# Kernel tuning notes

Hardware: AMD Instinct MI355X
Metric: run time of the kernel (lower is better)

## Reference

```python
import jax, jax.numpy as jnp
import numpy as np

N = 100000   # nodes
E = 600000   # edges
D = 128      # d_model
R = 200      # num_relations


def setup_inputs() -> dict:
    key = jax.random.key(0)
    ks = jax.random.split(key, 12)
    def nrm(k, shape, scale=0.02):
        return jax.random.normal(k, shape, jnp.float32) * scale
    return dict(
        node_features=jax.random.normal(ks[0], (N, D), jnp.float32),
        edge_index=jax.random.randint(ks[1], (2, E), 0, N),
        edge_type=jax.random.randint(ks[2], (E,), 0, R),
        rel_embed=nrm(ks[3], (R, D)),
        msg_w1=nrm(ks[4], (2 * D, D)), msg_b1=jnp.zeros((D,), jnp.float32),
        msg_w2=nrm(ks[5], (D, D)), msg_b2=jnp.zeros((D,), jnp.float32),
        attn_w1=nrm(ks[6], (2 * D, D)), attn_b1=jnp.zeros((D,), jnp.float32),
        attn_w2=nrm(ks[7], (D, 1)), attn_b2=jnp.zeros((1,), jnp.float32),
        ln1_g=jnp.ones((D,), jnp.float32), ln1_b=jnp.zeros((D,), jnp.float32),
        ffn_w1=nrm(ks[8], (D, 4 * D)), ffn_b1=jnp.zeros((4 * D,), jnp.float32),
        ffn_w2=nrm(ks[9], (4 * D, D)), ffn_b2=jnp.zeros((D,), jnp.float32),
        ln2_g=jnp.ones((D,), jnp.float32), ln2_b=jnp.zeros((D,), jnp.float32),
    )


def layer_norm(x, g, b, eps=1e-5):
    mu = x.mean(-1, keepdims=True)
    var = ((x - mu) ** 2).mean(-1, keepdims=True)
    return (x - mu) * jax.lax.rsqrt(var + eps) * g + b


def reference(node_features, edge_index, edge_type, rel_embed,
              msg_w1, msg_b1, msg_w2, msg_b2,
              attn_w1, attn_b1, attn_w2, attn_b2,
              ln1_g, ln1_b, ffn_w1, ffn_b1, ffn_w2, ffn_b2,
              ln2_g, ln2_b):
    Nn = node_features.shape[0]
    src, dst = edge_index[0], edge_index[1]
    # gather + edge message MLP
    src_feat = node_features[src]              # [E, D]
    rel_feat = rel_embed[edge_type]            # [E, D]
    h = jnp.concatenate([src_feat, rel_feat], axis=-1)          # [E, 2D]
    messages = jax.nn.relu(h @ msg_w1 + msg_b1) @ msg_w2 + msg_b2  # [E, D]
    # edge attention logits
    a_in = jnp.concatenate([node_features[dst], messages], axis=-1)  # [E, 2D]
    attn_raw = (jax.nn.leaky_relu(a_in @ attn_w1 + attn_b1, 0.2) @ attn_w2 + attn_b2)[:, 0]  # [E]
    # two-pass segment softmax over destination nodes
    attn_max = jax.ops.segment_max(attn_raw, dst, num_segments=Nn)   # [N]
    attn_exp = jnp.exp(attn_raw - attn_max[dst])                      # [E]
    attn_sum = jax.ops.segment_sum(attn_exp, dst, num_segments=Nn)   # [N]
    attn_w = attn_exp / (attn_sum[dst] + 1e-8)                        # [E]
    # scatter-add weighted messages
    aggr = jax.ops.segment_sum(attn_w[:, None] * messages, dst, num_segments=Nn)  # [N, D]
    x = layer_norm(node_features + aggr, ln1_g, ln1_b)
    ffn = jax.nn.gelu(x @ ffn_w1 + ffn_b1, approximate=False) @ ffn_w2 + ffn_b2
    return layer_norm(x + ffn, ln2_g, ln2_b)
```

## Files before the change

kernel.cpp:

```cpp
#include <hip/hip_runtime.h>
#include <hip/hip_bf16.h>

#define NN 100000
#define NE 600000
#define DD 128
#define RR 200
#define SCAN_NB ((NN + 255) / 256)

typedef __attribute__((ext_vector_type(8))) short bf16x8;
typedef __attribute__((ext_vector_type(4))) float f32x4;

__device__ __forceinline__ unsigned int bfbits(float x) {
    return (unsigned int)__builtin_bit_cast(unsigned short, __float2bfloat16(x));
}
__device__ __forceinline__ unsigned int pk2(float a, float b) {
    return bfbits(a) | (bfbits(b) << 16);
}
__device__ __forceinline__ unsigned short bf16s(float x) {
    return __builtin_bit_cast(unsigned short, __float2bfloat16(x));
}
__device__ __forceinline__ float unbf(unsigned short u) {
    return __builtin_bit_cast(float, ((unsigned int)u) << 16);
}
__device__ __forceinline__ float unlo(unsigned int u) {
    return __builtin_bit_cast(float, u << 16);
}
__device__ __forceinline__ float unhi(unsigned int u) {
    return __builtin_bit_cast(float, u & 0xffff0000u);
}

__device__ __forceinline__ void gload_lds16(const void* g, void* l) {
    __builtin_amdgcn_global_load_lds(
        (const __attribute__((address_space(1))) void*)g,
        (__attribute__((address_space(3))) void*)l, 16, 0, 0);
}

__global__ void k_initc(int* __restrict__ cnt) {
    int i = blockIdx.x * 256 + threadIdx.x;
    if (i < NN) cnt[i] = 0;
}

__global__ void k_hist(const int* __restrict__ dst, int* __restrict__ cnt) {
    int e = blockIdx.x * 256 + threadIdx.x;
    if (e < NE) atomicAdd(&cnt[dst[e]], 1);
}

__global__ void k_scanA(const int* __restrict__ cnt, int* __restrict__ bsum) {
    __shared__ int red[256];
    int i = blockIdx.x * 256 + threadIdx.x;
    red[threadIdx.x] = (i < NN) ? cnt[i] : 0;
    __syncthreads();
    for (int off = 128; off >= 1; off >>= 1) {
        if (threadIdx.x < off) red[threadIdx.x] += red[threadIdx.x + off];
        __syncthreads();
    }
    if (threadIdx.x == 0) bsum[blockIdx.x] = red[0];
}

__global__ void k_scanB(int* __restrict__ bsum) {
    __shared__ int sh[512];
    int t = threadIdx.x;
    int v = (t < SCAN_NB) ? bsum[t] : 0;
    sh[t] = v;
    __syncthreads();
    for (int off = 1; off < 512; off <<= 1) {
        int add = (t >= off) ? sh[t - off] : 0;
        __syncthreads();
        sh[t] += add;
        __syncthreads();
    }
    if (t < SCAN_NB) bsum[t] = sh[t] - v;
}

__global__ void k_scanC(const int* __restrict__ cnt, const int* __restrict__ bsum,
                        int* __restrict__ row_start, int* __restrict__ cursor) {
    __shared__ int sh[256];
    int i = blockIdx.x * 256 + threadIdx.x;
    int t = threadIdx.x;
    int v = (i < NN) ? cnt[i] : 0;
    sh[t] = v;
    __syncthreads();
    for (int off = 1; off < 256; off <<= 1) {
        int add = (t >= off) ? sh[t - off] : 0;
        __syncthreads();
        sh[t] += add;
        __syncthreads();
    }
    if (i < NN) {
        int ex = bsum[blockIdx.x] + sh[t] - v;
        row_start[i] = ex;
        cursor[i] = ex;
    }
}

__global__ void k_bucket(const int* __restrict__ src, const int* __restrict__ dst,
                         const int* __restrict__ etype, int* __restrict__ cursor,
                         int* __restrict__ srcs, int* __restrict__ ets,
                         int* __restrict__ dsts) {
    int e = blockIdx.x * 256 + threadIdx.x;
    if (e < NE) {
        int d = dst[e];
        int p = atomicAdd(&cursor[d], 1);
        srcs[p] = src[e];
        ets[p]  = etype[e];
        dsts[p] = d;
    }
}

__global__ void k_prep(const float* __restrict__ nf, unsigned short* __restrict__ nfb) {
    int i = blockIdx.x * 256 + threadIdx.x;
    if (i >= NN * DD / 8) return;
    const float* sp = nf + (size_t)i * 8;
    float4 f0 = *reinterpret_cast<const float4*>(sp);
    float4 f1 = *reinterpret_cast<const float4*>(sp + 4);
    uint4 v;
    v.x = pk2(f0.x, f0.y); v.y = pk2(f0.z, f0.w);
    v.z = pk2(f1.x, f1.y); v.w = pk2(f1.z, f1.w);
    *reinterpret_cast<uint4*>(nfb + (size_t)i * 8) = v;
}

__global__ void k_setup(const float* __restrict__ mw1, const float* __restrict__ mb1,
                        const float* __restrict__ mw2, const float* __restrict__ mb2,
                        const float* __restrict__ aw1, const float* __restrict__ rel,
                        const float* __restrict__ fw1, const float* __restrict__ fw2,
                        unsigned short* __restrict__ mw1p,
                        unsigned short* __restrict__ mw2p,
                        unsigned short* __restrict__ awTp,
                        unsigned short* __restrict__ mwBp,
                        unsigned short* __restrict__ fw1p,
                        unsigned short* __restrict__ fw2p,
                        unsigned short* __restrict__ relcb,
                        float* __restrict__ zb) {
    int idx = blockIdx.x * 256 + threadIdx.x;
    if (idx < 16384) {
        int i = idx & 7, l = (idx >> 3) & 63, ks = (idx >> 9) & 3, nt = idx >> 11;
        int k = ks * 32 + (l >> 4) * 8 + i, n = nt * 16 + (l & 15);
        mw1p[idx] = bf16s(mw1[k * 128 + n]);
    } else if (idx < 32768) {
        int j = idx - 16384;
        int i = j & 7, l = (j >> 3) & 63, ks = (j >> 9) & 3, nt = j >> 11;
        int k = ks * 32 + (l >> 4) * 8 + i, n = nt * 16 + (l & 15);
        mw2p[j] = bf16s(mw2[k * 128 + n]);
    } else if (idx < 49152) {
        int j = idx - 32768;
        int i = j & 7, l = (j >> 3) & 63, ks = (j >> 9) & 3, nt = j >> 11;
        int k = ks * 32 + (l >> 4) * 8 + i, n = nt * 16 + (l & 15);
        awTp[j] = bf16s(aw1[k * 128 + n]);
    } else if (idx < 65536) {
        int j = idx - 49152;
        int i = j & 7, l = (j >> 3) & 63, ks = (j >> 9) & 3, nt = j >> 11;
        int k = ks * 32 + (l >> 4) * 8 + i, n = nt * 16 + (l & 15);
        float s = 0.0f;
        for (int j2 = 0; j2 < 128; ++j2)
            s = fmaf(mw2[k * 128 + j2], aw1[(128 + j2) * 128 + n], s);
        mwBp[j] = bf16s(s);
    } else if (idx < 131072) {
        int j = idx - 65536;
        int i = j & 7, l = (j >> 3) & 63, ks = (j >> 9) & 3, nt = j >> 11;
        int k = ks * 32 + (l >> 4) * 8 + i, n = nt * 16 + (l & 15);
        fw1p[j] = bf16s(fw1[k * 512 + n]);
    } else if (idx < 196608) {
        int j = idx - 131072;
        int i = j & 7, l = (j >> 3) & 63, ks = (j >> 9) & 15, nt = j >> 13;
        int k = ks * 32 + (l >> 4) * 8 + i, n = nt * 16 + (l & 15);
        fw2p[j] = bf16s(fw2[k * 128 + n]);
    } else if (idx < 222208) {
        int j = idx - 196608;
        int r = j >> 7, n = j & 127;
        float s = mb1[n];
        for (int k = 0; k < 128; ++k)
            s = fmaf(rel[r * 128 + k], mw1[(128 + k) * 128 + n], s);
        relcb[j] = bf16s(s);
    } else if (idx < 222336) {
        int n = idx - 222208;
        float s = 0.0f;
        for (int j2 = 0; j2 < 128; ++j2)
            s = fmaf(mb2[j2], aw1[(128 + j2) * 128 + n], s);
        zb[n] = s;
    }
}

__global__ __launch_bounds__(256) void k_nfa(
    const unsigned short* __restrict__ nfb, const unsigned short* __restrict__ awTp,
    const float* __restrict__ ab1, unsigned short* __restrict__ nfa)
{
    __shared__ alignas(16) unsigned short XB[64 * 128];
    const int t = threadIdx.x;
    const int w = t >> 6, l = t & 63;
    const int wm = w >> 1, wn = w & 1;
    const int lm = l & 15, lk = l >> 4;
    const int lrow = l >> 4, lslot = l & 15;
    const int n0 = blockIdx.x * 64;

    #pragma unroll
    for (int it = 0; it < 4; ++it) {
        int rb = w * 16 + it * 4;
        int row = rb + lrow;
        long grow = n0 + row; if (grow >= NN) grow = NN - 1;
        int c = lslot ^ (row & 7);
        gload_lds16(nfb + grow * DD + c * 8, &XB[rb * 128]);
    }
    __syncthreads();

    f32x4 acc[2][4];
    #pragma unroll
    for (int mf = 0; mf < 2; ++mf)
        #pragma unroll
        for (int nfr = 0; nfr < 4; ++nfr) acc[mf][nfr] = (f32x4){0.f, 0.f, 0.f, 0.f};

    #pragma unroll
    for (int ks = 0; ks < 4; ++ks) {
        bf16x8 a[2];
        #pragma unroll
        for (int mf = 0; mf < 2; ++mf) {
            int m = wm * 32 + mf * 16 + lm;
            int slot = (ks * 4 + lk) ^ (m & 7);
            a[mf] = *reinterpret_cast<const bf16x8*>(&XB[m * 128 + slot * 8]);
        }
        #pragma unroll
        for (int nfr = 0; nfr < 4; ++nfr) {
            int nt = wn * 4 + nfr;
            bf16x8 b = *reinterpret_cast<const bf16x8*>(&awTp[((nt * 4 + ks) * 64 + l) * 8]);
            acc[0][nfr] = __builtin_amdgcn_mfma_f32_16x16x32_bf16(a[0], b, acc[0][nfr], 0, 0, 0);
            acc[1][nfr] = __builtin_amdgcn_mfma_f32_16x16x32_bf16(a[1], b, acc[1][nfr], 0, 0, 0);
        }
    }
    __syncthreads();

    #pragma unroll
    for (int nfr = 0; nfr < 4; ++nfr) {
        int n = wn * 64 + nfr * 16 + lm;
        float bv = ab1[n];
        #pragma unroll
        for (int mf = 0; mf < 2; ++mf)
            #pragma unroll
            for (int r = 0; r < 4; ++r) {
                int m = wm * 32 + mf * 16 + lk * 4 + r;
                XB[m * 128 + n] = bf16s(acc[mf][nfr][r] + bv);
            }
    }
    __syncthreads();

    #pragma unroll
    for (int j = 0; j < 4; ++j) {
        int q = j * 256 + t;
        int row = q >> 4, c16 = q & 15;
        if (n0 + row < NN)
            *reinterpret_cast<uint4*>(&nfa[(size_t)(n0 + row) * DD + c16 * 8]) =
                *reinterpret_cast<const uint4*>(&XB[row * 128 + c16 * 8]);
    }
}

__global__ __launch_bounds__(512) void k_edge(
    const unsigned short* __restrict__ nfb, const int* __restrict__ srcs,
    const int* __restrict__ dsts, const int* __restrict__ ets,
    const unsigned short* __restrict__ nfa, const unsigned short* __restrict__ relcb,
    const unsigned short* __restrict__ mw1p, const unsigned short* __restrict__ mwBp,
    const float* __restrict__ zb, const float* __restrict__ aw2,
    const float* __restrict__ ab2,
    unsigned short* __restrict__ hid_out, float* __restrict__ attn_raw)
{
    __shared__ alignas(16) unsigned short S[64 * 128];
    __shared__ alignas(16) unsigned short H[64 * 128];
    __shared__ float RED[64][4];

    const int t = threadIdx.x;
    const int w = t >> 6, l = t & 63;
    const int wm = w >> 2, wn = w & 3;
    const int lm = l & 15, lk = l >> 4;
    const int lrow = l >> 4, lslot = l & 15;
    const int e0 = blockIdx.x * 64;

    #pragma unroll
    for (int it = 0; it < 2; ++it) {
        int rb = w * 8 + it * 4;
        int row = rb + lrow;
        int c = lslot ^ (row & 7);
        gload_lds16(nfb + (size_t)srcs[e0 + row] * DD + c * 8, &S[rb * 128]);
    }
    #pragma unroll
    for (int it = 0; it < 2; ++it) {
        int rb = w * 8 + it * 4;
        int row = rb + lrow;
        int c = lslot ^ (row & 7);
        gload_lds16(relcb + (size_t)ets[e0 + row] * DD + c * 8, &H[rb * 128]);
    }
    __syncthreads();

    {
        f32x4 acc1[2][2];
        #pragma unroll
        for (int mf = 0; mf < 2; ++mf)
            #pragma unroll
            for (int nfr = 0; nfr < 2; ++nfr) acc1[mf][nfr] = (f32x4){0.f, 0.f, 0.f, 0.f};

        #pragma unroll
        for (int ks = 0; ks < 4; ++ks) {
            bf16x8 a[2];
            #pragma unroll
            for (int mf = 0; mf < 2; ++mf) {
                int m = wm * 32 + mf * 16 + lm;
                int slot = (ks * 4 + lk) ^ (m & 7);
                a[mf] = *reinterpret_cast<const bf16x8*>(&S[m * 128 + slot * 8]);
            }
            #pragma unroll
            for (int nfr = 0; nfr < 2; ++nfr) {
                int nt = wn * 2 + nfr;
                bf16x8 b = *reinterpret_cast<const bf16x8*>(&mw1p[((nt * 4 + ks) * 64 + l) * 8]);
                acc1[0][nfr] = __builtin_amdgcn_mfma_f32_16x16x32_bf16(a[0], b, acc1[0][nfr], 0, 0, 0);
                acc1[1][nfr] = __builtin_amdgcn_mfma_f32_16x16x32_bf16(a[1], b, acc1[1][nfr], 0, 0, 0);
            }
        }
        #pragma unroll
        for (int nfr = 0; nfr < 2; ++nfr) {
            int n = (wn * 2 + nfr) * 16 + lm;
            #pragma unroll
            for (int mf = 0; mf < 2; ++mf)
                #pragma unroll
                for (int r = 0; r < 4; ++r) {
                    int m = wm * 32 + mf * 16 + lk * 4 + r;
                    int sl = m * 128 + ((n >> 3) ^ (m & 7)) * 8 + (n & 7);
                    float v = acc1[mf][nfr][r] + unbf(H[sl]);
                    v = fmaxf(v, 0.0f);
                    H[sl] = bf16s(v);
                }
        }
    }
    __syncthreads();

    #pragma unroll
    for (int j = 0; j < 2; ++j) {
        int q = j * 512 + t;
        int row = q >> 4, c16 = q & 15;
        int slot = c16 ^ (row & 7);
        *reinterpret_cast<uint4*>(&hid_out[(size_t)(e0 + row) * DD + c16 * 8]) =
            *reinterpret_cast<const uint4*>(&H[row * 128 + slot * 8]);
    }
    #pragma unroll
    for (int it = 0; it < 2; ++it) {
        int rb = w * 8 + it * 4;
        int row = rb + lrow;
        int c = lslot ^ (row & 7);
        gload_lds16(nfa + (size_t)dsts[e0 + row] * DD + c * 8, &S[rb * 128]);
    }

    f32x4 acc[2][2];
    #pragma unroll
    for (int mf = 0; mf < 2; ++mf)
        #pragma unroll
        for (int nfr = 0; nfr < 2; ++nfr) acc[mf][nfr] = (f32x4){0.f, 0.f, 0.f, 0.f};

    #pragma unroll
    for (int ks = 0; ks < 4; ++ks) {
        bf16x8 a[2];
        #pragma unroll
        for (int mf = 0; mf < 2; ++mf) {
            int m = wm * 32 + mf * 16 + lm;
            int slot = (ks * 4 + lk) ^ (m & 7);
            a[mf] = *reinterpret_cast<const bf16x8*>(&H[m * 128 + slot * 8]);
        }
        #pragma unroll
        for (int nfr = 0; nfr < 2; ++nfr) {
            int nt = wn * 2 + nfr;
            bf16x8 b = *reinterpret_cast<const bf16x8*>(&mwBp[((nt * 4 + ks) * 64 + l) * 8]);
            acc[0][nfr] = __builtin_amdgcn_mfma_f32_16x16x32_bf16(a[0], b, acc[0][nfr], 0, 0, 0);
            acc[1][nfr] = __builtin_amdgcn_mfma_f32_16x16x32_bf16(a[1], b, acc[1][nfr], 0, 0, 0);
        }
    }
    __syncthreads();

    {
        float zbv[2], aw2v[2];
        #pragma unroll
        for (int nfr = 0; nfr < 2; ++nfr) {
            int nc = (wn * 2 + nfr) * 16 + lm;
            zbv[nfr] = zb[nc];
            aw2v[nfr] = aw2[nc];
        }
        #pragma unroll
        for (int mf = 0; mf < 2; ++mf)
            #pragma unroll
            for (int r = 0; r < 4; ++r) {
                int m = wm * 32 + mf * 16 + lk * 4 + r;
                float s = 0.0f;
                #pragma unroll
                for (int nfr = 0; nfr < 2; ++nfr) {
                    int nc = (wn * 2 + nfr) * 16 + lm;
                    float v = acc[mf][nfr][r] + zbv[nfr]
                            + unbf(S[m * 128 + ((nc >> 3) ^ (m & 7)) * 8 + (nc & 7)]);
                    v = (v > 0.0f) ? v : 0.2f * v;
                    s = fmaf(v, aw2v[nfr], s);
                }
                s += __shfl_xor(s, 1, 64);
                s += __shfl_xor(s, 2, 64);
                s += __shfl_xor(s, 4, 64);
                s += __shfl_xor(s, 8, 64);
                if (lm == 0) RED[m][wn] = s;
            }
    }
    __syncthreads();

    if (t < 64) {
        attn_raw[e0 + t] = RED[t][0] + RED[t][1] + RED[t][2] + RED[t][3] + ab2[0];
    }
}

__global__ __launch_bounds__(256) void k_aggr(
    const unsigned short* __restrict__ hid, const float* __restrict__ raw,
    const int* __restrict__ row_start, const int* __restrict__ cnt,
    unsigned short* __restrict__ haggrb)
{
    const int l = threadIdx.x & 63;
    const int n = blockIdx.x * 4 + (threadIdx.x >> 6);
    if (n >= NN) return;
    const int rs = row_start[n], deg = cnt[n];

    float m = -INFINITY;
    for (int j = l; j < deg; j += 64) m = fmaxf(m, raw[rs + j]);
    #pragma unroll
    for (int off = 32; off >= 1; off >>= 1) m = fmaxf(m, __shfl_xor(m, off, 64));

    float s = 0.0f;
    for (int j = l; j < deg; j += 64) s += expf(raw[rs + j] - m);
    #pragma unroll
    for (int off = 32; off >= 1; off >>= 1) s += __shfl_xor(s, off, 64);
    const float rinv = 1.0f / (s + 1e-8f);

    float a0 = 0.0f, a1 = 0.0f;
    for (int j = 0; j < deg; ++j) {
        float w = expf(raw[rs + j] - m) * rinv;
        unsigned int v = *reinterpret_cast<const unsigned int*>(
            &hid[(size_t)(rs + j) * DD + l * 2]);
        a0 = fmaf(w, unlo(v), a0);
        a1 = fmaf(w, unhi(v), a1);
    }
    *reinterpret_cast<unsigned int*>(&haggrb[(size_t)n * DD + l * 2]) = pk2(a0, a1);
}

__global__ __launch_bounds__(512) void k_node(
    const float* __restrict__ nf, const unsigned short* __restrict__ haggrb,
    const unsigned short* __restrict__ mw2p, const float* __restrict__ mb2,
    const float* __restrict__ g1, const float* __restrict__ b1,
    const unsigned short* __restrict__ fw1p, const float* __restrict__ fb1,
    const unsigned short* __restrict__ fw2p, const float* __restrict__ fb2,
    const float* __restrict__ g2, const float* __restrict__ b2,
    float* __restrict__ out)
{
    __shared__ alignas(16) unsigned short XB[64 * 128];
    __shared__ alignas(16) unsigned short HB[64 * 256];

    const int t = threadIdx.x;
    const int w = t >> 6, l = t & 63;
    const int wm = w >> 2, wn = w & 3;
    const int lm = l & 15, lk = l >> 4;
    const int lrow = l >> 4, lslot = l & 15;
    const int row = t >> 3;
    const int q = t & 7;
    const long n0 = (long)blockIdx.x * 64;
    const long rg = n0 + row;
    const long rc = (rg < NN) ? rg : (NN - 1);

    unsigned short* HG = HB;
    #pragma unroll
    for (int it = 0; it < 2; ++it) {
        int rb = w * 8 + it * 4;
        int rr = rb + lrow;
        long grow = n0 + rr; if (grow >= NN) grow = NN - 1;
        int c = lslot ^ (rr & 7);
        gload_lds16(haggrb + grow * DD + c * 8, &HG[rb * 128]);
    }
    __syncthreads();

    {
        f32x4 acc0[2][2];
        #pragma unroll
        for (int mf = 0; mf < 2; ++mf)
            #pragma unroll
            for (int nfr = 0; nfr < 2; ++nfr) acc0[mf][nfr] = (f32x4){0.f, 0.f, 0.f, 0.f};

        #pragma unroll
        for (int ks = 0; ks < 4; ++ks) {
            bf16x8 a[2];
            #pragma unroll
            for (int mf = 0; mf < 2; ++mf) {
                int m = wm * 32 + mf * 16 + lm;
                int slot = (ks * 4 + lk) ^ (m & 7);
                a[mf] = *reinterpret_cast<const bf16x8*>(&HG[m * 128 + slot * 8]);
            }
            #pragma unroll
            for (int nfr = 0; nfr < 2; ++nfr) {
                int nt = wn * 2 + nfr;
                bf16x8 b = *reinterpret_cast<const bf16x8*>(&mw2p[((nt * 4 + ks) * 64 + l) * 8]);
                acc0[0][nfr] = __builtin_amdgcn_mfma_f32_16x16x32_bf16(a[0], b, acc0[0][nfr], 0, 0, 0);
                acc0[1][nfr] = __builtin_amdgcn_mfma_f32_16x16x32_bf16(a[1], b, acc0[1][nfr], 0, 0, 0);
            }
        }
        #pragma unroll
        for (int nfr = 0; nfr < 2; ++nfr) {
            int n = (wn * 2 + nfr) * 16 + lm;
            float bv = mb2[n];
            #pragma unroll
            for (int mf = 0; mf < 2; ++mf)
                #pragma unroll
                for (int r = 0; r < 4; ++r) {
                    int m = wm * 32 + mf * 16 + lk * 4 + r;
                    XB[m * 128 + ((n >> 3) ^ (m & 7)) * 8 + (n & 7)] = bf16s(acc0[mf][nfr][r] + bv);
                }
        }
    }
    __syncthreads();

    float xr[16];
    float s = 0.0f, ss = 0.0f;
    {
        const float* xp = nf + rc * DD + q * 16;
        #pragma unroll
        for (int i = 0; i < 2; ++i) {
            int c = q * 2 + i, slot = c ^ (row & 7);
            uint4 v = *reinterpret_cast<const uint4*>(&XB[row * 128 + slot * 8]);
            float f[8];
            f[0] = unlo(v.x); f[1] = unhi(v.x); f[2] = unlo(v.y); f[3] = unhi(v.y);
            f[4] = unlo(v.z); f[5] = unhi(v.z); f[6] = unlo(v.w); f[7] = unhi(v.w);
            float4 a = *reinterpret_cast<const float4*>(xp + i * 8);
            float4 b = *reinterpret_cast<const float4*>(xp + i * 8 + 4);
            float vv[8] = {a.x + f[0], a.y + f[1], a.z + f[2], a.w + f[3],
                           b.x + f[4], b.y + f[5], b.z + f[6], b.w + f[7]};
            #pragma unroll
            for (int j = 0; j < 8; ++j) {
                xr[i * 8 + j] = vv[j];
                s += vv[j];
                ss = fmaf(vv[j], vv[j], ss);
            }
        }
    }
    s  += __shfl_xor(s, 1, 64);  s  += __shfl_xor(s, 2, 64);  s  += __shfl_xor(s, 4, 64);
    ss += __shfl_xor(ss, 1, 64); ss += __shfl_xor(ss, 2, 64); ss += __shfl_xor(ss, 4, 64);
    {
        float mu = s * (1.0f / DD);
        float var = ss * (1.0f / DD) - mu * mu;
        float rstd = rsqrtf(var + 1e-5f);
        #pragma unroll
        for (int i = 0; i < 4; ++i) {
            float4 gv = *reinterpret_cast<const float4*>(g1 + q * 16 + i * 4);
            float4 bv = *reinterpret_cast<const float4*>(b1 + q * 16 + i * 4);
            xr[i * 4 + 0] = (xr[i * 4 + 0] - mu) * rstd * gv.x + bv.x;
            xr[i * 4 + 1] = (xr[i * 4 + 1] - mu) * rstd * gv.y + bv.y;
            xr[i * 4 + 2] = (xr[i * 4 + 2] - mu) * rstd * gv.z + bv.z;
            xr[i * 4 + 3] = (xr[i * 4 + 3] - mu) * rstd * gv.w + bv.w;
        }
        #pragma unroll
        for (int i = 0; i < 2; ++i) {
            int c = q * 2 + i, slot = c ^ (row & 7);
            uint4 v;
            v.x = pk2(xr[i * 8 + 0], xr[i * 8 + 1]);
            v.y = pk2(xr[i * 8 + 2], xr[i * 8 + 3]);
            v.z = pk2(xr[i * 8 + 4], xr[i * 8 + 5]);
            v.w = pk2(xr[i * 8 + 6], xr[i * 8 + 7]);
            *reinterpret_cast<uint4*>(&XB[row * 128 + slot * 8]) = v;
        }
    }
    __syncthreads();

    f32x4 acc2[2][2];
    #pragma unroll
    for (int mf = 0; mf < 2; ++mf)
        #pragma unroll
        for (int nfr = 0; nfr < 2; ++nfr) acc2[mf][nfr] = (f32x4){0.f, 0.f, 0.f, 0.f};

    #pragma unroll
    for (int half = 0; half < 2; ++half) {
        f32x4 acc[2][4];
        #pragma unroll
        for (int mf = 0; mf < 2; ++mf)
            #pragma unroll
            for (int nfr = 0; nfr < 4; ++nfr) acc[mf][nfr] = (f32x4){0.f, 0.f, 0.f, 0.f};

        #pragma unroll
        for (int ks = 0; ks < 4; ++ks) {
            bf16x8 a[2];
            #pragma unroll
            for (int mf = 0; mf < 2; ++mf) {
                int m = wm * 32 + mf * 16 + lm;
                int slot = (ks * 4 + lk) ^ (m & 7);
                a[mf] = *reinterpret_cast<const bf16x8*>(&XB[m * 128 + slot * 8]);
            }
            #pragma unroll
            for (int nfr = 0; nfr < 4; ++nfr) {
                int nt = half * 16 + wn * 4 + nfr;
                bf16x8 b = *reinterpret_cast<const bf16x8*>(&fw1p[((nt * 4 + ks) * 64 + l) * 8]);
                acc[0][nfr] = __builtin_amdgcn_mfma_f32_16x16x32_bf16(a[0], b, acc[0][nfr], 0, 0, 0);
                acc[1][nfr] = __builtin_amdgcn_mfma_f32_16x16x32_bf16(a[1], b, acc[1][nfr], 0, 0, 0);
            }
        }
        #pragma unroll
        for (int nfr = 0; nfr < 4; ++nfr) {
            int nl = (wn * 4 + nfr) * 16 + lm;
            float bv = fb1[half * 256 + nl];
            #pragma unroll
            for (int mf = 0; mf < 2; ++mf)
                #pragma unroll
                for (int r = 0; r < 4; ++r) {
                    int m = wm * 32 + mf * 16 + lk * 4 + r;
                    float h = acc[mf][nfr][r] + bv;
                    float e = __expf(h * -1.702f);
                    float gvv = h * __builtin_amdgcn_rcpf(1.0f + e);
                    HB[m * 256 + (((nl >> 3) ^ (m & 7)) * 8) + (nl & 7)] = bf16s(gvv);
                }
        }
        __syncthreads();

        #pragma unroll
        for (int ks = 0; ks < 8; ++ks) {
            bf16x8 a[2];
            #pragma unroll
            for (int mf = 0; mf < 2; ++mf) {
                int m = wm * 32 + mf * 16 + lm;
                int slot = (ks * 4 + lk) ^ (m & 7);
                a[mf] = *reinterpret_cast<const bf16x8*>(&HB[m * 256 + slot * 8]);
            }
            #pragma unroll
            for (int nfr = 0; nfr < 2; ++nfr) {
                int nt = wn * 2 + nfr;
                int kg = half * 8 + ks;
                bf16x8 b = *reinterpret_cast<const bf16x8*>(&fw2p[((nt * 16 + kg) * 64 + l) * 8]);
                acc2[0][nfr] = __builtin_amdgcn_mfma_f32_16x16x32_bf16(a[0], b, acc2[0][nfr], 0, 0, 0);
                acc2[1][nfr] = __builtin_amdgcn_mfma_f32_16x16x32_bf16(a[1], b, acc2[1][nfr], 0, 0, 0);
            }
        }
        __syncthreads();
    }

    #pragma unroll
    for (int nfr = 0; nfr < 2; ++nfr) {
        int n = (wn * 2 + nfr) * 16 + lm;
        float bv = fb2[n];
        #pragma unroll
        for (int mf = 0; mf < 2; ++mf)
            #pragma unroll
            for (int r = 0; r < 4; ++r) {
                int m = wm * 32 + mf * 16 + lk * 4 + r;
                XB[m * 128 + (((n >> 3) ^ (m & 7)) * 8) + (n & 7)] = bf16s(acc2[mf][nfr][r] + bv);
            }
    }
    __syncthreads();

    float s2 = 0.0f, ss2 = 0.0f;
    #pragma unroll
    for (int i = 0; i < 2; ++i) {
        int c = q * 2 + i, slot = c ^ (row & 7);
        uint4 v = *reinterpret_cast<const uint4*>(&XB[row * 128 + slot * 8]);
        float f[8];
        f[0] = unlo(v.x); f[1] = unhi(v.x); f[2] = unlo(v.y); f[3] = unhi(v.y);
        f[4] = unlo(v.z); f[5] = unhi(v.z); f[6] = unlo(v.w); f[7] = unhi(v.w);
        #pragma unroll
        for (int j = 0; j < 8; ++j) {
            float vv = xr[i * 8 + j] + f[j];
            xr[i * 8 + j] = vv;
            s2 += vv;
            ss2 = fmaf(vv, vv, ss2);
        }
    }
    s2  += __shfl_xor(s2, 1, 64);  s2  += __shfl_xor(s2, 2, 64);  s2  += __shfl_xor(s2, 4, 64);
    ss2 += __shfl_xor(ss2, 1, 64); ss2 += __shfl_xor(ss2, 2, 64); ss2 += __shfl_xor(ss2, 4, 64);
    {
        float mu = s2 * (1.0f / DD);
        float var = ss2 * (1.0f / DD) - mu * mu;
        float rstd = rsqrtf(var + 1e-5f);
        if (rg < NN) {
            float* op = out + rg * DD + q * 16;
            #pragma unroll
            for (int i = 0; i < 4; ++i) {
                float4 gv = *reinterpret_cast<const float4*>(g2 + q * 16 + i * 4);
                float4 bv = *reinterpret_cast<const float4*>(b2 + q * 16 + i * 4);
                float4 o;
                o.x = (xr[i * 4 + 0] - mu) * rstd * gv.x + bv.x;
                o.y = (xr[i * 4 + 1] - mu) * rstd * gv.y + bv.y;
                o.z = (xr[i * 4 + 2] - mu) * rstd * gv.z + bv.z;
                o.w = (xr[i * 4 + 3] - mu) * rstd * gv.w + bv.w;
                *reinterpret_cast<float4*>(op + i * 4) = o;
            }
        }
    }
}

extern "C" void kernel_launch(void* const* d_in, const int* in_sizes, int n_in,
                              void* d_out, int out_size, void* d_ws, size_t ws_size,
                              hipStream_t stream)
{
    const float* nf  = (const float*)d_in[0];
    const int*   ei  = (const int*)d_in[1];
    const int*   et  = (const int*)d_in[2];
    const float* rel = (const float*)d_in[3];
    const float* mw1 = (const float*)d_in[4];
    const float* mb1 = (const float*)d_in[5];
    const float* mw2 = (const float*)d_in[6];
    const float* mb2 = (const float*)d_in[7];
    const float* aw1 = (const float*)d_in[8];
    const float* ab1 = (const float*)d_in[9];
    const float* aw2 = (const float*)d_in[10];
    const float* ab2 = (const float*)d_in[11];
    const float* g1  = (const float*)d_in[12];
    const float* b1  = (const float*)d_in[13];
    const float* fw1 = (const float*)d_in[14];
    const float* fb1 = (const float*)d_in[15];
    const float* fw2 = (const float*)d_in[16];
    const float* fb2 = (const float*)d_in[17];
    const float* g2  = (const float*)d_in[18];
    const float* b2  = (const float*)d_in[19];
    float* out = (float*)d_out;

    char* ws = (char*)d_ws;
    size_t off = 0;
    auto alloc = [&](size_t bytes) -> char* {
        char* p = ws + off;
        off += (bytes + 255) & ~(size_t)255;
        return p;
    };
    unsigned short* hid = (unsigned short*)alloc((size_t)NE * DD * 2);
    float* attn_raw = (float*)alloc((size_t)NE * 4);
    unsigned short* haggrb = (unsigned short*)alloc((size_t)NN * DD * 2);
    unsigned short* nfb  = (unsigned short*)alloc((size_t)NN * DD * 2);
    unsigned short* relcb = (unsigned short*)alloc((size_t)RR * DD * 2);
    float* zb  = (float*)alloc((size_t)128 * 4);
    int* cnt       = (int*)alloc((size_t)NN * 4);
    int* row_start = (int*)alloc((size_t)NN * 4);
    int* cursor    = (int*)alloc((size_t)NN * 4);
    int* srcs      = (int*)alloc((size_t)NE * 4);
    int* ets       = (int*)alloc((size_t)NE * 4);
    int* dsts      = (int*)alloc((size_t)NE * 4);
    int* bsum      = (int*)alloc((size_t)SCAN_NB * 4);
    unsigned short* mw1p = (unsigned short*)alloc(16384 * 2);
    unsigned short* mw2p = (unsigned short*)alloc(16384 * 2);
    unsigned short* awTp = (unsigned short*)alloc(16384 * 2);
    unsigned short* mwBp = (unsigned short*)alloc(16384 * 2);
    unsigned short* fw1p = (unsigned short*)alloc(65536 * 2);
    unsigned short* fw2p = (unsigned short*)alloc(65536 * 2);

    unsigned short* nfa = haggrb;

    const int* srcp = ei;
    const int* dstp = ei + NE;

    hipLaunchKernelGGL(k_initc, dim3(SCAN_NB), dim3(256), 0, stream, cnt);
    hipLaunchKernelGGL(k_hist, dim3((NE + 255) / 256), dim3(256), 0, stream, dstp, cnt);
    hipLaunchKernelGGL(k_scanA, dim3(SCAN_NB), dim3(256), 0, stream, cnt, bsum);
    hipLaunchKernelGGL(k_scanB, dim3(1), dim3(512), 0, stream, bsum);
    hipLaunchKernelGGL(k_scanC, dim3(SCAN_NB), dim3(256), 0, stream, cnt, bsum, row_start, cursor);
    hipLaunchKernelGGL(k_bucket, dim3((NE + 255) / 256), dim3(256), 0, stream,
                       srcp, dstp, et, cursor, srcs, ets, dsts);
    hipLaunchKernelGGL(k_prep, dim3(NN * DD / 8 / 256), dim3(256), 0, stream, nf, nfb);
    hipLaunchKernelGGL(k_setup, dim3(869), dim3(256), 0, stream,
                       mw1, mb1, mw2, mb2, aw1, rel, fw1, fw2,
                       mw1p, mw2p, awTp, mwBp, fw1p, fw2p, relcb, zb);
    hipLaunchKernelGGL(k_nfa, dim3((NN + 63) / 64), dim3(256), 0, stream,
                       nfb, awTp, ab1, nfa);
    hipLaunchKernelGGL(k_edge, dim3(NE / 64), dim3(512), 0, stream,
                       nfb, srcs, dsts, ets, nfa, relcb,
                       mw1p, mwBp, zb, aw2, ab2,
                       hid, attn_raw);
    hipLaunchKernelGGL(k_aggr, dim3((NN + 3) / 4), dim3(256), 0, stream,
                       hid, attn_raw, row_start, cnt, haggrb);
    hipLaunchKernelGGL(k_node, dim3((NN + 63) / 64), dim3(512), 0, stream,
                       nf, haggrb, mw2p, mb2, g1, b1, fw1p, fb1, fw2p, fb2, g2, b2, out);
}
```

Before: 432.2 us.

## Fuse bf16 conversion into node-attention GEMM and aggregation into node kernel

Result: slower. 589.9 us (+36.5%).

```diff
diff --git a/kernel.cpp b/kernel.cpp
--- a/kernel.cpp
+++ b/kernel.cpp
@@ -105,18 +105,6 @@
         ets[p]  = etype[e];
         dsts[p] = d;
     }
-}
-
-__global__ void k_prep(const float* __restrict__ nf, unsigned short* __restrict__ nfb) {
-    int i = blockIdx.x * 256 + threadIdx.x;
-    if (i >= NN * DD / 8) return;
-    const float* sp = nf + (size_t)i * 8;
-    float4 f0 = *reinterpret_cast<const float4*>(sp);
-    float4 f1 = *reinterpret_cast<const float4*>(sp + 4);
-    uint4 v;
-    v.x = pk2(f0.x, f0.y); v.y = pk2(f0.z, f0.w);
-    v.z = pk2(f1.x, f1.y); v.w = pk2(f1.z, f1.w);
-    *reinterpret_cast<uint4*>(nfb + (size_t)i * 8) = v;
 }
 
 __global__ void k_setup(const float* __restrict__ mw1, const float* __restrict__ mb1,
@@ -180,25 +168,40 @@
     }
 }
 
-__global__ __launch_bounds__(256) void k_nfa(
-    const unsigned short* __restrict__ nfb, const unsigned short* __restrict__ awTp,
-    const float* __restrict__ ab1, unsigned short* __restrict__ nfa)
+__global__ __launch_bounds__(256) void k_prepnfa(
+    const float* __restrict__ nf, const unsigned short* __restrict__ awTp,
+    const float* __restrict__ ab1,
+    unsigned short* __restrict__ nfb, unsigned short* __restrict__ nfa)
 {
     __shared__ alignas(16) unsigned short XB[64 * 128];
     const int t = threadIdx.x;
     const int w = t >> 6, l = t & 63;
     const int wm = w >> 1, wn = w & 1;
     const int lm = l & 15, lk = l >> 4;
-    const int lrow = l >> 4, lslot = l & 15;
     const int n0 = blockIdx.x * 64;
 
-    #pragma unroll
-    for (int it = 0; it < 4; ++it) {
-        int rb = w * 16 + it * 4;
-        int row = rb + lrow;
-        long grow = n0 + row; if (grow >= NN) grow = NN - 1;
-        int c = lslot ^ (row & 7);
-        gload_lds16(nfb + grow * DD + c * 8, &XB[rb * 128]);
+    {
+        const int row = t >> 2, seg = t & 3;
+        long ng = n0 + row; if (ng >= NN) ng = NN - 1;
+        const float* sp = nf + ng * DD + seg * 32;
+        uint4 o[4];
+        #pragma unroll
+        for (int i = 0; i < 4; ++i) {
+            float4 f0 = *reinterpret_cast<const float4*>(sp + i * 8);
+            float4 f1 = *reinterpret_cast<const float4*>(sp + i * 8 + 4);
+            o[i].x = pk2(f0.x, f0.y); o[i].y = pk2(f0.z, f0.w);
+            o[i].z = pk2(f1.x, f1.y); o[i].w = pk2(f1.z, f1.w);
+        }
+        if (n0 + row < NN) {
+            #pragma unroll
+            for (int i = 0; i < 4; ++i)
+                *reinterpret_cast<uint4*>(&nfb[(size_t)(n0 + row) * DD + (seg * 4 + i) * 8]) = o[i];
+        }
+        #pragma unroll
+        for (int i = 0; i < 4; ++i) {
+            int c = seg * 4 + i, slot = c ^ (row & 7);
+            *reinterpret_cast<uint4*>(&XB[row * 128 + slot * 8]) = o[i];
+        }
     }
     __syncthreads();
 
@@ -405,40 +408,10 @@
     }
 }
 
-__global__ __launch_bounds__(256) void k_aggr(
-    const unsigned short* __restrict__ hid, const float* __restrict__ raw,
-    const int* __restrict__ row_start, const int* __restrict__ cnt,
-    unsigned short* __restrict__ haggrb)
-{
-    const int l = threadIdx.x & 63;
-    const int n = blockIdx.x * 4 + (threadIdx.x >> 6);
-    if (n >= NN) return;
-    const int rs = row_start[n], deg = cnt[n];
-
-    float m = -INFINITY;
-    for (int j = l; j < deg; j += 64) m = fmaxf(m, raw[rs + j]);
-    #pragma unroll
-    for (int off = 32; off >= 1; off >>= 1) m = fmaxf(m, __shfl_xor(m, off, 64));
-
-    float s = 0.0f;
-    for (int j = l; j < deg; j += 64) s += expf(raw[rs + j] - m);
-    #pragma unroll
-    for (int off = 32; off >= 1; off >>= 1) s += __shfl_xor(s, off, 64);
-    const float rinv = 1.0f / (s + 1e-8f);
-
-    float a0 = 0.0f, a1 = 0.0f;
-    for (int j = 0; j < deg; ++j) {
-        float w = expf(raw[rs + j] - m) * rinv;
-        unsigned int v = *reinterpret_cast<const unsigned int*>(
-            &hid[(size_t)(rs + j) * DD + l * 2]);
-        a0 = fmaf(w, unlo(v), a0);
-        a1 = fmaf(w, unhi(v), a1);
-    }
-    *reinterpret_cast<unsigned int*>(&haggrb[(size_t)n * DD + l * 2]) = pk2(a0, a1);
-}
-
 __global__ __launch_bounds__(512) void k_node(
-    const float* __restrict__ nf, const unsigned short* __restrict__ haggrb,
+    const float* __restrict__ nf, const unsigned short* __restrict__ hid,
+    const float* __restrict__ raw, const int* __restrict__ row_start,
+    const int* __restrict__ cnt,
     const unsigned short* __restrict__ mw2p, const float* __restrict__ mb2,
     const float* __restrict__ g1, const float* __restrict__ b1,
     const unsigned short* __restrict__ fw1p, const float* __restrict__ fb1,
@@ -453,7 +426,6 @@
     const int w = t >> 6, l = t & 63;
     const int wm = w >> 2, wn = w & 3;
     const int lm = l & 15, lk = l >> 4;
-    const int lrow = l >> 4, lslot = l & 15;
     const int row = t >> 3;
     const int q = t & 7;
     const long n0 = (long)blockIdx.x * 64;
@@ -461,13 +433,34 @@
     const long rc = (rg < NN) ? rg : (NN - 1);
 
     unsigned short* HG = HB;
-    #pragma unroll
-    for (int it = 0; it < 2; ++it) {
-        int rb = w * 8 + it * 4;
-        int rr = rb + lrow;
-        long grow = n0 + rr; if (grow >= NN) grow = NN - 1;
-        int c = lslot ^ (rr & 7);
-        gload_lds16(haggrb + grow * DD + c * 8, &HG[rb * 128]);
+
+    #pragma unroll 1
+    for (int i = 0; i < 8; ++i) {
+        int nl = w * 8 + i;
+        long ng = n0 + nl;
+        float a0 = 0.0f, a1 = 0.0f;
+        if (ng < NN) {
+            int rs = row_start[ng], deg = cnt[ng];
+            float m = -INFINITY;
+            for (int j = l; j < deg; j += 64) m = fmaxf(m, raw[rs + j]);
+            #pragma unroll
+            for (int off = 32; off >= 1; off >>= 1) m = fmaxf(m, __shfl_xor(m, off, 64));
+            float s = 0.0f;
+            for (int j = l; j < deg; j += 64) s += expf(raw[rs + j] - m);
+            #pragma unroll
+            for (int off = 32; off >= 1; off >>= 1) s += __shfl_xor(s, off, 64);
+            const float rinv = 1.0f / (s + 1e-8f);
+            for (int j = 0; j < deg; ++j) {
+                float wj = expf(raw[rs + j] - m) * rinv;
+                unsigned int v = *reinterpret_cast<const unsigned int*>(
+                    &hid[(size_t)(rs + j) * DD + l * 2]);
+                a0 = fmaf(wj, unlo(v), a0);
+                a1 = fmaf(wj, unhi(v), a1);
+            }
+        }
+        int c = l >> 2;
+        int slot = c ^ (nl & 7);
+        *reinterpret_cast<unsigned int*>(&HG[nl * 128 + slot * 8 + ((l * 2) & 7)]) = pk2(a0, a1);
     }
     __syncthreads();
 
@@ -718,8 +711,8 @@
     };
     unsigned short* hid = (unsigned short*)alloc((size_t)NE * DD * 2);
     float* attn_raw = (float*)alloc((size_t)NE * 4);
-    unsigned short* haggrb = (unsigned short*)alloc((size_t)NN * DD * 2);
-    unsigned short* nfb  = (unsigned short*)alloc((size_t)NN * DD * 2);
+    unsigned short* nfa = (unsigned short*)alloc((size_t)NN * DD * 2);
+    unsigned short* nfb = (unsigned short*)alloc((size_t)NN * DD * 2);
     unsigned short* relcb = (unsigned short*)alloc((size_t)RR * DD * 2);
     float* zb  = (float*)alloc((size_t)128 * 4);
     int* cnt       = (int*)alloc((size_t)NN * 4);
@@ -736,8 +729,6 @@
     unsigned short* fw1p = (unsigned short*)alloc(65536 * 2);
     unsigned short* fw2p = (unsigned short*)alloc(65536 * 2);
 
-    unsigned short* nfa = haggrb;
-
     const int* srcp = ei;
     const int* dstp = ei + NE;
 
@@ -748,18 +739,16 @@
     hipLaunchKernelGGL(k_scanC, dim3(SCAN_NB), dim3(256), 0, stream, cnt, bsum, row_start, cursor);
     hipLaunchKernelGGL(k_bucket, dim3((NE + 255) / 256), dim3(256), 0, stream,
                        srcp, dstp, et, cursor, srcs, ets, dsts);
-    hipLaunchKernelGGL(k_prep, dim3(NN * DD / 8 / 256), dim3(256), 0, stream, nf, nfb);
     hipLaunchKernelGGL(k_setup, dim3(869), dim3(256), 0, stream,
                        mw1, mb1, mw2, mb2, aw1, rel, fw1, fw2,
                        mw1p, mw2p, awTp, mwBp, fw1p, fw2p, relcb, zb);
-    hipLaunchKernelGGL(k_nfa, dim3((NN + 63) / 64), dim3(256), 0, stream,
-                       nfb, awTp, ab1, nfa);
+    hipLaunchKernelGGL(k_prepnfa, dim3((NN + 63) / 64), dim3(256), 0, stream,
+                       nf, awTp, ab1, nfb, nfa);
     hipLaunchKernelGGL(k_edge, dim3(NE / 64), dim3(512), 0, stream,
                        nfb, srcs, dsts, ets, nfa, relcb,
                        mw1p, mwBp, zb, aw2, ab2,
                        hid, attn_raw);
-    hipLaunchKernelGGL(k_aggr, dim3((NN + 3) / 4), dim3(256), 0, stream,
-                       hid, attn_raw, row_start, cnt, haggrb);
     hipLaunchKernelGGL(k_node, dim3((NN + 63) / 64), dim3(512), 0, stream,
-                       nf, haggrb, mw2p, mb2, g1, b1, fw1p, fb1, fw2p, fb2, g2, b2, out);
-}
+                       nf, hid, attn_raw, row_start, cnt,
+                       mw2p, mb2, g1, b1, fw1p, fb1, fw2p, fb2, g2, b2, out);
+}
```
